# Kernel tuning notes

Hardware: AMD Instinct MI355X
Metric: run time of the kernel (lower is better)

The kernel has to match this reference:

```python
import jax, jax.numpy as jnp
import numpy as np

N, T, B, NI, NO = 1024, 512, 128, 6, 2
ALPHA = 0.1          # dt/tau = 1/10
SIGMA_REC = 0.03
SIGMA_INP = 0.03
GAMMA = 0.1
D = 0.0
SLOPE = 1.0          # relu activation slope


def setup_inputs() -> dict:
    key = jax.random.key(0)
    ks = jax.random.split(key, 6)
    u = jax.random.normal(ks[0], (NI, T, B), jnp.float32)
    rec_noise = jax.random.normal(ks[1], (N, T, B), jnp.float32)
    inp_noise = jax.random.normal(ks[2], (NI, T, B), jnp.float32)
    # recurrent weights ~ N(0, 1/N) scaled to spectral radius ~1.2, zero diagonal
    W_rec = jax.random.normal(ks[3], (N, N), jnp.float32) * (1.2 / np.sqrt(N))
    W_rec = W_rec - jnp.diag(jnp.diag(W_rec))
    W_inp = jax.random.normal(ks[4], (N, NI), jnp.float32) / np.sqrt(N)
    W_out = jax.random.normal(ks[5], (NO, N), jnp.float32) / np.sqrt(N)
    y_init = jnp.zeros((N,), jnp.float32)
    return dict(u=u, rec_noise=rec_noise, inp_noise=inp_noise,
                W_rec=W_rec, W_inp=W_inp, W_out=W_out, y_init=y_init)


def _run(u, rec_noise, inp_noise, W_rec, W_inp, W_out, y_init):
    inp_scale = jnp.sqrt(2.0 / ALPHA) * SIGMA_INP
    rec_scale = jnp.sqrt(2.0 / ALPHA) * SIGMA_REC
    s0 = jnp.broadcast_to(y_init[:, None], (N, B))
    # time-major slices for scan; Euler loop runs T-1 steps (state[0] = y_init)
    u_t = jnp.moveaxis(u[:, : T - 1, :], 1, 0)            # (T-1, NI, B)
    in_t = jnp.moveaxis(inp_noise[:, : T - 1, :], 1, 0)   # (T-1, NI, B)
    rn_t = jnp.moveaxis(rec_noise[:, : T - 1, :], 1, 0)   # (T-1, N, B)

    def step(s, xs):
        ut, it, rt = xs
        h = W_rec @ s + W_inp @ (ut + inp_scale * it)      # (N, B)
        rhs = -(s - D) + jnp.maximum(0.0, SLOPE * h) + rec_scale * rt - GAMMA * s ** 3
        s_new = s + ALPHA * rhs
        return s_new, s_new

    _, states_rest = jax.lax.scan(step, s0, (u_t, in_t, rn_t))
    states = jnp.concatenate([s0[None], states_rest], axis=0)  # (T, N, B)
    outputs = jnp.einsum('on,tnb->otb', W_out, states)         # (NO, T, B)
    return outputs


def reference(u, rec_noise, inp_noise, W_rec, W_inp, W_out, y_init):
    return _run(u, rec_noise, inp_noise, W_rec, W_inp, W_out, y_init)
```

## Files before the change

### kernel.cpp

```cpp
#include <hip/hip_runtime.h>

typedef float f32x4 __attribute__((ext_vector_type(4)));
typedef short bf16x8 __attribute__((ext_vector_type(8)));

#define N_  1024
#define T_  512
#define B_  128
#define NI_ 6
#define NO_ 2
#define NS_ 0.13416407864998738f
#define ALPHA_ 0.1f
#define GAMMA_ 0.1f

#define NG   16
#define CPG  8
#define RPB  64
#define SBG  (CPG * N_)
#define SBT  (NG * SBG)
#define FSTRIDE 16
#define PSTR 1032
#define PWS  1025

#define MFMA_(A,B,C) __builtin_amdgcn_mfma_f32_16x16x32_bf16(A,B,C,0,0,0)

#define PIN_WF() asm volatile("" \
    : "+v"(wh[0]),"+v"(wh[1]),"+v"(wh[2]),"+v"(wh[3]),"+v"(wh[4]),"+v"(wh[5]),"+v"(wh[6]),"+v"(wh[7]), \
      "+v"(wl[0]),"+v"(wl[1]),"+v"(wl[2]),"+v"(wl[3]),"+v"(wl[4]),"+v"(wl[5]),"+v"(wl[6]),"+v"(wl[7]))

__device__ __forceinline__ unsigned short f2bf(float f) {
    unsigned x = __float_as_uint(f);
    return (unsigned short)((x + 0x7fffu + ((x >> 16) & 1u)) >> 16);
}
__device__ __forceinline__ float bf2f(unsigned short h) {
    return __uint_as_float(((unsigned)h) << 16);
}
__device__ __forceinline__ void st_sys_u(unsigned* p, unsigned v) {
    asm volatile("global_store_dword %0, %1, off sc0 sc1" :: "v"(p), "v"(v) : "memory");
}
__device__ __forceinline__ unsigned ld_flag(const unsigned* p) {
    unsigned v;
    asm volatile("global_load_dword %0, %1, off sc0 sc1\n\t"
                 "s_waitcnt vmcnt(0)"
                 : "=v"(v) : "v"(p) : "memory");
    return v;
}

__global__ __launch_bounds__(1024, 4) void rnn_kernel(
    const float* __restrict__ u,
    const float* __restrict__ rn,
    const float* __restrict__ ino,
    const float* __restrict__ Wrec,
    const float* __restrict__ Winp,
    const float* __restrict__ Wout,
    const float* __restrict__ yinit,
    float* __restrict__ out,
    unsigned int* __restrict__ flags,
    unsigned int* __restrict__ sbuf)
{
    __shared__ __align__(16) unsigned short shP[2][CPG][PSTR];
    __shared__ float pw[CPG * PWS];
    __shared__ float outL[NO_ * T_ * CPG];
    __shared__ float rnL[RPB * 9];
    __shared__ float uL[NI_ * CPG];
    __shared__ float inoL[NI_ * CPG];
    __shared__ float WinpL[RPB * 7];
    __shared__ float WoutL[NO_ * RPB];

    const int bid  = blockIdx.x;
    const int g    = bid >> 4;
    const int R    = bid & 15;
    const int col0 = g * CPG;
    const int r0   = R * RPB;
    const int tid  = threadIdx.x;
    const int wv   = tid >> 6;
    const int ln   = tid & 63;
    const int k0   = wv * 64;
    const int lq   = ln >> 4;
    const int lm   = ln & 15;
    const int cc   = ln & 7;
    const int tid3 = tid - 512;

    bf16x8 wh[8], wl[8];
    #pragma unroll
    for (int mt = 0; mt < 4; ++mt)
      #pragma unroll
      for (int kt = 0; kt < 2; ++kt) {
        const float* wr = Wrec + (size_t)(r0 + mt*16 + lm) * N_ + (k0 + kt*32 + lq*8);
        bf16x8 h8, l8;
        #pragma unroll
        for (int j = 0; j < 8; ++j) {
            const float v = wr[j];
            const unsigned short hb = f2bf(v);
            const unsigned short lb = f2bf(v - bf2f(hb));
            h8[j] = (short)hb; l8[j] = (short)lb;
        }
        wh[mt*2+kt] = h8; wl[mt*2+kt] = l8;
      }
    PIN_WF();

    if (tid < RPB * NI_) {
        const int r = tid / NI_, q = tid % NI_;
        WinpL[r * 7 + q] = Winp[(r0 + r) * NI_ + q];
    }
    if (tid < NO_ * RPB)
        WoutL[tid] = Wout[(tid >> 6) * N_ + r0 + (tid & 63)];

    {
        const float yv = yinit[k0 + ln];
        const unsigned short hb = f2bf(yv);
        const unsigned short lb = f2bf(yv - bf2f(hb));
        #pragma unroll
        for (int c = 0; c < CPG; ++c) { shP[0][c][k0 + ln] = hb; shP[1][c][k0 + ln] = lb; }
    }

    float s_prev = (wv < 8) ? yinit[r0 + ln] : 0.f;

    float pfa = 0.f, pfb = 0.f;
    if (tid3 >= 0) {
        pfa = rn[(size_t)(r0 + (tid3 >> 3)) * (T_ * B_) + col0 + (tid3 & 7)];
        if (tid3 < 2 * NI_ * CPG) {
            const int q = (tid3 >> 3) % NI_, pc = tid3 & 7;
            pfb = ((tid3 < NI_ * CPG) ? u : ino)[q * (T_ * B_) + col0 + pc];
        }
    }
    __syncthreads();

    if (wv < 8) {
        #pragma unroll
        for (int o = 0; o < NO_; ++o) {
            float pp = WoutL[o * RPB + ln] * s_prev;
            #pragma unroll
            for (int off = 32; off; off >>= 1) pp += __shfl_down(pp, off, 64);
            if (ln == 0) outL[(o << 12) | wv] = pp;
        }
    }

    #pragma unroll 1
    for (int t = 0; t < T_ - 1; ++t) {
        PIN_WF();
        if (tid3 >= 0) {
            rnL[(tid3 >> 3) * 9 + (tid3 & 7)] = pfa;
            if (tid3 < NI_ * CPG)          uL[tid3] = pfb;
            else if (tid3 < 2 * NI_ * CPG) inoL[tid3 - NI_ * CPG] = pfb;
        }

        f32x4 acc[4] = {{0,0,0,0},{0,0,0,0},{0,0,0,0},{0,0,0,0}};
        #pragma unroll
        for (int kt = 0; kt < 2; ++kt) {
            const bf16x8 bh = *(const bf16x8*)&shP[0][cc][k0 + kt*32 + lq*8];
            const bf16x8 bl = *(const bf16x8*)&shP[1][cc][k0 + kt*32 + lq*8];
            #pragma unroll
            for (int mt = 0; mt < 4; ++mt) {
                acc[mt] = MFMA_(wh[mt*2+kt], bh, acc[mt]);
                acc[mt] = MFMA_(wh[mt*2+kt], bl, acc[mt]);
                acc[mt] = MFMA_(wl[mt*2+kt], bh, acc[mt]);
                acc[mt] = MFMA_(wl[mt*2+kt], bl, acc[mt]);
            }
        }
        if (lm < 8) {
            #pragma unroll
            for (int mt = 0; mt < 4; ++mt)
                #pragma unroll
                for (int rg = 0; rg < 4; ++rg)
                    pw[lm * PWS + wv * 64 + mt * 16 + lq * 4 + rg] = acc[mt][rg];
        }
        __syncthreads();

        const bool notlast = (t < T_ - 2);
        unsigned* sbn = sbuf + (size_t)((t + 1) & 1) * SBT + (size_t)g * SBG;

        if (wv < 8) {
            float hs = 0.f;
            #pragma unroll
            for (int w2 = 0; w2 < 16; ++w2) hs += pw[wv * PWS + w2 * 64 + ln];
            #pragma unroll
            for (int q = 0; q < NI_; ++q)
                hs = fmaf(WinpL[ln * 7 + q],
                          fmaf(NS_, inoL[q * CPG + wv], uL[q * CPG + wv]), hs);
            const float rhs  = -s_prev + fmaxf(0.f, hs) + NS_ * rnL[ln * 9 + wv]
                               - GAMMA_ * s_prev * s_prev * s_prev;
            const float snew = fmaf(ALPHA_, rhs, s_prev);
            s_prev = snew;
            const unsigned short hb = f2bf(snew);
            const unsigned short lb = f2bf(snew - bf2f(hb));
            if (notlast) st_sys_u(&sbn[wv * N_ + r0 + ln], ((unsigned)hb << 16) | lb);
            float po0 = WoutL[ln] * snew;
            float po1 = WoutL[RPB + ln] * snew;
            #pragma unroll
            for (int off = 32; off; off >>= 1) {
                po0 += __shfl_down(po0, off, 64);
                po1 += __shfl_down(po1, off, 64);
            }
            if (notlast) {
                asm volatile("s_waitcnt vmcnt(0)" ::: "memory");
                if (ln == 0)
                    __hip_atomic_fetch_add(&flags[(size_t)(g * 16 + R) * FSTRIDE], 1u,
                                           __ATOMIC_RELAXED, __HIP_MEMORY_SCOPE_AGENT);
            }
            if (ln == 0) {
                outL[(0 << 12) | ((t + 1) << 3) | wv] = po0;
                outL[(1 << 12) | ((t + 1) << 3) | wv] = po1;
            }
        }

        if (tid3 >= 0 && notlast) {
            pfa = rn[(size_t)(r0 + (tid3 >> 3)) * (T_ * B_)
                     + (size_t)(t + 1) * B_ + col0 + (tid3 & 7)];
            if (tid3 < 2 * NI_ * CPG) {
                const int q = (tid3 >> 3) % NI_, pc = tid3 & 7;
                pfb = ((tid3 < NI_ * CPG) ? u : ino)
                          [q * (T_ * B_) + (t + 1) * B_ + col0 + pc];
            }
        }

        if (notlast) {
            const unsigned tgt = 8u * (unsigned)(t + 1);
            const unsigned* flp = flags + (size_t)(g * 16 + wv) * FSTRIDE;
            while (ld_flag(flp) < tgt) __builtin_amdgcn_s_sleep(1);
            const unsigned* P0 = sbn + k0 + ln;
            unsigned d0,d1,d2,d3,d4,d5,d6,d7;
            asm volatile(
                "global_load_dword %0, %8, off sc0 sc1\n\t"
                "global_load_dword %1, %9, off sc0 sc1\n\t"
                "global_load_dword %2, %10, off sc0 sc1\n\t"
                "global_load_dword %3, %11, off sc0 sc1\n\t"
                "global_load_dword %4, %12, off sc0 sc1\n\t"
                "global_load_dword %5, %13, off sc0 sc1\n\t"
                "global_load_dword %6, %14, off sc0 sc1\n\t"
                "global_load_dword %7, %15, off sc0 sc1\n\t"
                "s_waitcnt vmcnt(0)"
                : "=&v"(d0),"=&v"(d1),"=&v"(d2),"=&v"(d3),
                  "=&v"(d4),"=&v"(d5),"=&v"(d6),"=&v"(d7)
                : "v"(P0), "v"(P0 + N_), "v"(P0 + 2*N_), "v"(P0 + 3*N_),
                  "v"(P0 + 4*N_), "v"(P0 + 5*N_), "v"(P0 + 6*N_), "v"(P0 + 7*N_)
                : "memory");
            shP[0][0][k0+ln] = (unsigned short)(d0 >> 16); shP[1][0][k0+ln] = (unsigned short)(d0 & 0xffffu);
            shP[0][1][k0+ln] = (unsigned short)(d1 >> 16); shP[1][1][k0+ln] = (unsigned short)(d1 & 0xffffu);
            shP[0][2][k0+ln] = (unsigned short)(d2 >> 16); shP[1][2][k0+ln] = (unsigned short)(d2 & 0xffffu);
            shP[0][3][k0+ln] = (unsigned short)(d3 >> 16); shP[1][3][k0+ln] = (unsigned short)(d3 & 0xffffu);
            shP[0][4][k0+ln] = (unsigned short)(d4 >> 16); shP[1][4][k0+ln] = (unsigned short)(d4 & 0xffffu);
            shP[0][5][k0+ln] = (unsigned short)(d5 >> 16); shP[1][5][k0+ln] = (unsigned short)(d5 & 0xffffu);
            shP[0][6][k0+ln] = (unsigned short)(d6 >> 16); shP[1][6][k0+ln] = (unsigned short)(d6 & 0xffffu);
            shP[0][7][k0+ln] = (unsigned short)(d7 >> 16); shP[1][7][k0+ln] = (unsigned short)(d7 & 0xffffu);
        }
        __syncthreads();
    }

    __syncthreads();
    #pragma unroll
    for (int i = 0; i < 8; ++i) {
        const int j = tid + i * 1024;
        const int o = j >> 12, tt = (j >> 3) & (T_ - 1), c = j & 7;
        atomicAdd(&out[(size_t)o * (T_ * B_) + (size_t)tt * B_ + col0 + c], outL[j]);
    }
}

extern "C" void kernel_launch(void* const* d_in, const int* in_sizes, int n_in,
                              void* d_out, int out_size, void* d_ws, size_t ws_size,
                              hipStream_t stream) {
    const float* u    = (const float*)d_in[0];
    const float* rn   = (const float*)d_in[1];
    const float* ino  = (const float*)d_in[2];
    const float* Wrec = (const float*)d_in[3];
    const float* Winp = (const float*)d_in[4];
    const float* Wout = (const float*)d_in[5];
    const float* yin  = (const float*)d_in[6];
    float* out = (float*)d_out;

    unsigned int* flags = (unsigned int*)d_ws;
    unsigned int* sbuf  = (unsigned int*)((char*)d_ws + 32768);

    hipMemsetAsync(d_ws, 0, 32768, stream);
    hipMemsetAsync(d_out, 0, (size_t)out_size * sizeof(float), stream);

    void* args[] = {(void*)&u, (void*)&rn, (void*)&ino, (void*)&Wrec, (void*)&Winp,
                    (void*)&Wout, (void*)&yin, (void*)&out, (void*)&flags, (void*)&sbuf};
    hipLaunchCooperativeKernel((void*)rnn_kernel, dim3(256), dim3(1024), args, 0, stream);
}
```

Baseline: 2.581 ms.

## Load state fragments directly into MFMA registers and aggregate per-block flag signals

Removes the shared-memory staging buffer for the recurrent state. Each wave now loads its MFMA B-fragments straight from the global exchange buffer with dwordx4 loads and repacks the hi/lo bf16 halves in registers. The matmul for the next step is moved to right after the spin-wait, so it completes before the block barrier. Per-wave global flag increments are replaced by an LDS counter, and only the last wave of a block bumps the global flag once, which cuts atomic traffic and changes the polling target. Input prefetch is moved after the MFMA, adding latency to that load but shortening the critical path of the cross-block exchange.

```diff
diff --git a/kernel.cpp b/kernel.cpp
--- a/kernel.cpp
+++ b/kernel.cpp
@@ -2,6 +2,7 @@
 
 typedef float f32x4 __attribute__((ext_vector_type(4)));
 typedef short bf16x8 __attribute__((ext_vector_type(8)));
+typedef unsigned u32x4 __attribute__((ext_vector_type(4)));
 
 #define N_  1024
 #define T_  512
@@ -18,7 +19,6 @@
 #define SBG  (CPG * N_)
 #define SBT  (NG * SBG)
 #define FSTRIDE 16
-#define PSTR 1032
 #define PWS  1025
 
 #define MFMA_(A,B,C) __builtin_amdgcn_mfma_f32_16x16x32_bf16(A,B,C,0,0,0)
@@ -44,6 +44,34 @@
                  : "=v"(v) : "v"(p) : "memory");
     return v;
 }
+
+union FragU { u32x4 u; bf16x8 v; };
+__device__ __forceinline__ void mkfrag(u32x4 a, u32x4 b, bf16x8& hi, bf16x8& lo) {
+    FragU h, l;
+    h.u[0] = (a[1] & 0xFFFF0000u) | (a[0] >> 16);
+    h.u[1] = (a[3] & 0xFFFF0000u) | (a[2] >> 16);
+    h.u[2] = (b[1] & 0xFFFF0000u) | (b[0] >> 16);
+    h.u[3] = (b[3] & 0xFFFF0000u) | (b[2] >> 16);
+    l.u[0] = (a[1] << 16) | (a[0] & 0xFFFFu);
+    l.u[1] = (a[3] << 16) | (a[2] & 0xFFFFu);
+    l.u[2] = (b[1] << 16) | (b[0] & 0xFFFFu);
+    l.u[3] = (b[3] << 16) | (b[2] & 0xFFFFu);
+    hi = h.v; lo = l.v;
+}
+
+#define DO_MFMA() do { \
+    _Pragma("unroll") \
+    for (int mt_ = 0; mt_ < 4; ++mt_) { \
+        acc[mt_] = MFMA_(wh[mt_*2+0], bh0, acc[mt_]); \
+        acc[mt_] = MFMA_(wh[mt_*2+0], bl0, acc[mt_]); \
+        acc[mt_] = MFMA_(wl[mt_*2+0], bh0, acc[mt_]); \
+        acc[mt_] = MFMA_(wl[mt_*2+0], bl0, acc[mt_]); \
+        acc[mt_] = MFMA_(wh[mt_*2+1], bh1, acc[mt_]); \
+        acc[mt_] = MFMA_(wh[mt_*2+1], bl1, acc[mt_]); \
+        acc[mt_] = MFMA_(wl[mt_*2+1], bh1, acc[mt_]); \
+        acc[mt_] = MFMA_(wl[mt_*2+1], bl1, acc[mt_]); \
+    } \
+} while (0)
 
 __global__ __launch_bounds__(1024, 4) void rnn_kernel(
     const float* __restrict__ u,
@@ -57,7 +85,6 @@
     unsigned int* __restrict__ flags,
     unsigned int* __restrict__ sbuf)
 {
-    __shared__ __align__(16) unsigned short shP[2][CPG][PSTR];
     __shared__ float pw[CPG * PWS];
     __shared__ float outL[NO_ * T_ * CPG];
     __shared__ float rnL[RPB * 9];
@@ -65,6 +92,7 @@
     __shared__ float inoL[NI_ * CPG];
     __shared__ float WinpL[RPB * 7];
     __shared__ float WoutL[NO_ * RPB];
+    __shared__ unsigned scnt;
 
     const int bid  = blockIdx.x;
     const int g    = bid >> 4;
@@ -104,14 +132,7 @@
     }
     if (tid < NO_ * RPB)
         WoutL[tid] = Wout[(tid >> 6) * N_ + r0 + (tid & 63)];
-
-    {
-        const float yv = yinit[k0 + ln];
-        const unsigned short hb = f2bf(yv);
-        const unsigned short lb = f2bf(yv - bf2f(hb));
-        #pragma unroll
-        for (int c = 0; c < CPG; ++c) { shP[0][c][k0 + ln] = hb; shP[1][c][k0 + ln] = lb; }
-    }
+    if (tid == 0) scnt = 0u;
 
     float s_prev = (wv < 8) ? yinit[r0 + ln] : 0.f;
 
@@ -133,6 +154,31 @@
             for (int off = 32; off; off >>= 1) pp += __shfl_down(pp, off, 64);
             if (ln == 0) outL[(o << 12) | wv] = pp;
         }
+    }
+
+    f32x4 acc[4] = {{0,0,0,0},{0,0,0,0},{0,0,0,0},{0,0,0,0}};
+    {
+        u32x4 a0, b0, a1, b1;
+        #pragma unroll
+        for (int j2 = 0; j2 < 4; ++j2) {
+            #pragma unroll
+            for (int kt = 0; kt < 2; ++kt) {
+                const int base = k0 + kt * 32 + lq * 8;
+                const float v0 = yinit[base + 2*j2];
+                const float v1 = yinit[base + 2*j2 + 1];
+                unsigned short h0 = f2bf(v0), h1 = f2bf(v1);
+                unsigned w0 = ((unsigned)h0 << 16) | f2bf(v0 - bf2f(h0));
+                unsigned w1 = ((unsigned)h1 << 16) | f2bf(v1 - bf2f(h1));
+                if (j2 < 2) { if (kt == 0) { a0[2*j2] = w0; a0[2*j2+1] = w1; }
+                              else        { a1[2*j2] = w0; a1[2*j2+1] = w1; } }
+                else        { if (kt == 0) { b0[2*(j2-2)] = w0; b0[2*(j2-2)+1] = w1; }
+                              else        { b1[2*(j2-2)] = w0; b1[2*(j2-2)+1] = w1; } }
+            }
+        }
+        bf16x8 bh0, bl0, bh1, bl1;
+        mkfrag(a0, b0, bh0, bl0);
+        mkfrag(a1, b1, bh1, bl1);
+        DO_MFMA();
     }
 
     #pragma unroll 1
@@ -143,20 +189,6 @@
             if (tid3 < NI_ * CPG)          uL[tid3] = pfb;
             else if (tid3 < 2 * NI_ * CPG) inoL[tid3 - NI_ * CPG] = pfb;
         }
-
-        f32x4 acc[4] = {{0,0,0,0},{0,0,0,0},{0,0,0,0},{0,0,0,0}};
-        #pragma unroll
-        for (int kt = 0; kt < 2; ++kt) {
-            const bf16x8 bh = *(const bf16x8*)&shP[0][cc][k0 + kt*32 + lq*8];
-            const bf16x8 bl = *(const bf16x8*)&shP[1][cc][k0 + kt*32 + lq*8];
-            #pragma unroll
-            for (int mt = 0; mt < 4; ++mt) {
-                acc[mt] = MFMA_(wh[mt*2+kt], bh, acc[mt]);
-                acc[mt] = MFMA_(wh[mt*2+kt], bl, acc[mt]);
-                acc[mt] = MFMA_(wl[mt*2+kt], bh, acc[mt]);
-                acc[mt] = MFMA_(wl[mt*2+kt], bl, acc[mt]);
-            }
-        }
         if (lm < 8) {
             #pragma unroll
             for (int mt = 0; mt < 4; ++mt)
@@ -168,6 +200,8 @@
 
         const bool notlast = (t < T_ - 2);
         unsigned* sbn = sbuf + (size_t)((t + 1) & 1) * SBT + (size_t)g * SBG;
+        const unsigned tgt = (unsigned)(t + 1);
+        const unsigned* flp = flags + (size_t)(g * 16 + wv) * FSTRIDE;
 
         if (wv < 8) {
             float hs = 0.f;
@@ -193,9 +227,12 @@
             }
             if (notlast) {
                 asm volatile("s_waitcnt vmcnt(0)" ::: "memory");
-                if (ln == 0)
-                    __hip_atomic_fetch_add(&flags[(size_t)(g * 16 + R) * FSTRIDE], 1u,
-                                           __ATOMIC_RELAXED, __HIP_MEMORY_SCOPE_AGENT);
+                if (ln == 0) {
+                    unsigned old = atomicAdd(&scnt, 1u);
+                    if (old == 8u * (unsigned)t + 7u)
+                        __hip_atomic_fetch_add(&flags[(size_t)(g * 16 + R) * FSTRIDE],
+                                               1u, __ATOMIC_RELAXED, __HIP_MEMORY_SCOPE_AGENT);
+                }
             }
             if (ln == 0) {
                 outL[(0 << 12) | ((t + 1) << 3) | wv] = po0;
@@ -203,45 +240,36 @@
             }
         }
 
-        if (tid3 >= 0 && notlast) {
-            pfa = rn[(size_t)(r0 + (tid3 >> 3)) * (T_ * B_)
-                     + (size_t)(t + 1) * B_ + col0 + (tid3 & 7)];
-            if (tid3 < 2 * NI_ * CPG) {
-                const int q = (tid3 >> 3) % NI_, pc = tid3 & 7;
-                pfb = ((tid3 < NI_ * CPG) ? u : ino)
-                          [q * (T_ * B_) + (t + 1) * B_ + col0 + pc];
-            }
-        }
-
         if (notlast) {
-            const unsigned tgt = 8u * (unsigned)(t + 1);
-            const unsigned* flp = flags + (size_t)(g * 16 + wv) * FSTRIDE;
             while (ld_flag(flp) < tgt) __builtin_amdgcn_s_sleep(1);
-            const unsigned* P0 = sbn + k0 + ln;
-            unsigned d0,d1,d2,d3,d4,d5,d6,d7;
+
+            const unsigned* up = sbn + cc * N_ + k0 + lq * 8;
+            u32x4 q0, q1, q2, q3;
             asm volatile(
-                "global_load_dword %0, %8, off sc0 sc1\n\t"
-                "global_load_dword %1, %9, off sc0 sc1\n\t"
-                "global_load_dword %2, %10, off sc0 sc1\n\t"
-                "global_load_dword %3, %11, off sc0 sc1\n\t"
-                "global_load_dword %4, %12, off sc0 sc1\n\t"
-                "global_load_dword %5, %13, off sc0 sc1\n\t"
-                "global_load_dword %6, %14, off sc0 sc1\n\t"
-                "global_load_dword %7, %15, off sc0 sc1\n\t"
+                "global_load_dwordx4 %0, %4, off sc0 sc1\n\t"
+                "global_load_dwordx4 %1, %4, off offset:16 sc0 sc1\n\t"
+                "global_load_dwordx4 %2, %4, off offset:128 sc0 sc1\n\t"
+                "global_load_dwordx4 %3, %4, off offset:144 sc0 sc1\n\t"
                 "s_waitcnt vmcnt(0)"
-                : "=&v"(d0),"=&v"(d1),"=&v"(d2),"=&v"(d3),
-                  "=&v"(d4),"=&v"(d5),"=&v"(d6),"=&v"(d7)
-                : "v"(P0), "v"(P0 + N_), "v"(P0 + 2*N_), "v"(P0 + 3*N_),
-                  "v"(P0 + 4*N_), "v"(P0 + 5*N_), "v"(P0 + 6*N_), "v"(P0 + 7*N_)
-                : "memory");
-            shP[0][0][k0+ln] = (unsigned short)(d0 >> 16); shP[1][0][k0+ln] = (unsigned short)(d0 & 0xffffu);
-            shP[0][1][k0+ln] = (unsigned short)(d1 >> 16); shP[1][1][k0+ln] = (unsigned short)(d1 & 0xffffu);
-            shP[0][2][k0+ln] = (unsigned short)(d2 >> 16); shP[1][2][k0+ln] = (unsigned short)(d2 & 0xffffu);
-            shP[0][3][k0+ln] = (unsigned short)(d3 >> 16); shP[1][3][k0+ln] = (unsigned short)(d3 & 0xffffu);
-            shP[0][4][k0+ln] = (unsigned short)(d4 >> 16); shP[1][4][k0+ln] = (unsigned short)(d4 & 0xffffu);
-            shP[0][5][k0+ln] = (unsigned short)(d5 >> 16); shP[1][5][k0+ln] = (unsigned short)(d5 & 0xffffu);
-            shP[0][6][k0+ln] = (unsigned short)(d6 >> 16); shP[1][6][k0+ln] = (unsigned short)(d6 & 0xffffu);
-            shP[0][7][k0+ln] = (unsigned short)(d7 >> 16); shP[1][7][k0+ln] = (unsigned short)(d7 & 0xffffu);
+                : "=&v"(q0), "=&v"(q1), "=&v"(q2), "=&v"(q3)
+                : "v"(up) : "memory");
+            bf16x8 bh0, bl0, bh1, bl1;
+            mkfrag(q0, q1, bh0, bl0);
+            mkfrag(q2, q3, bh1, bl1);
+
+            #pragma unroll
+            for (int mt = 0; mt < 4; ++mt) acc[mt] = (f32x4){0,0,0,0};
+            DO_MFMA();
+
+            if (tid3 >= 0) {
+                pfa = rn[(size_t)(r0 + (tid3 >> 3)) * (T_ * B_)
+                         + (size_t)(t + 1) * B_ + col0 + (tid3 & 7)];
+                if (tid3 < 2 * NI_ * CPG) {
+                    const int q = (tid3 >> 3) % NI_, pc = tid3 & 7;
+                    pfb = ((tid3 < NI_ * CPG) ? u : ino)
+                              [q * (T_ * B_) + (t + 1) * B_ + col0 + pc];
+                }
+            }
         }
         __syncthreads();
     }
```

Result: no change. 2.601 ms (+0.8%).
